# Kernel tuning notes

Measured on AMD Instinct MI355X. Metric: run time of the kernel, lower is better.

Reference implementation:

```python
import jax, jax.numpy as jnp
import numpy as np

N_NODES = 50000
N_EDGES = 1_600_000
T = 2
F_IN = 128
F_OUT = 128


def setup_inputs() -> dict:
    key = jax.random.key(0)
    k1, k2, k3, k4, k5, k6 = jax.random.split(key, 6)
    node_features = jax.random.normal(k1, (N_NODES, T, F_IN), dtype=jnp.float32)
    edge_weights = jax.random.uniform(k2, (T, N_EDGES), dtype=jnp.float32)
    src = jax.random.randint(k3, (N_EDGES,), 0, N_NODES, dtype=jnp.int32)
    dst = jax.random.randint(k4, (N_EDGES,), 0, N_NODES, dtype=jnp.int32)
    W = jax.random.normal(k5, (F_OUT, F_IN), dtype=jnp.float32) / np.sqrt(F_IN)
    b = jax.random.normal(k6, (F_OUT,), dtype=jnp.float32) * 0.01
    return {"node_features": node_features, "edge_weights": edge_weights,
            "src": src, "dst": dst, "W": W, "b": b}


def reference(node_features, edge_weights, src, dst, W, b):
    # DGL: graph.edata['e'] = edge_weights.t().unsqueeze(-1)  -> [E, T, 1]
    w = jnp.transpose(edge_weights)[:, :, None]          # [E, T, 1]
    # u_mul_e: gather src node features, scale by edge weight -> [E, T, F]
    msg = node_features[src] * w
    # sum aggregation at destination nodes -> [N, T, F]
    h = jax.ops.segment_sum(msg, dst, num_segments=node_features.shape[0])
    # Linear(in_features, out_features) with bias
    return jnp.einsum('ntf,of->nto', h, W) + b
```

## Files before the change

kernel.cpp:

```cpp
#include <hip/hip_runtime.h>
#include <hip/hip_bf16.h>
#include <hip/hip_fp16.h>


#define TBLOCK 256
#define CAP 96
#define NGRP 8

typedef unsigned int  uint2_v  __attribute__((ext_vector_type(2)));
typedef float         float4_v __attribute__((ext_vector_type(4)));

#define SWZ(r) ((((r) + ((r) >> 2))) & 7)

__global__ void __launch_bounds__(TBLOCK)
transform_kernel(const float* __restrict__ x, const float* __restrict__ W,
                 __half* __restrict__ y, int nrows) {
    __shared__ float xs[64 * 128];
    __shared__ float Wsh[64 * 128];

    const int tid = threadIdx.x;
    const int tc = tid & 15, tr = tid >> 4;
    const int rowbase = (blockIdx.x >> 1) * 64;
    const int colbase = (blockIdx.x & 1) << 6;

    for (int p = tid; p < 2048; p += TBLOCK) {
        int oL = p >> 5, fb = p & 31;
        *(float4*)&Wsh[oL * 128 + (fb ^ SWZ(oL)) * 4] =
            *(const float4*)&W[((size_t)(colbase + oL)) * 128 + fb * 4];
    }
    for (int p = tid; p < 2048; p += TBLOCK) {
        int r = p >> 5, fb = p & 31;
        int row = rowbase + r;
        float4 v = make_float4(0.f, 0.f, 0.f, 0.f);
        if (row < nrows) v = *(const float4*)&x[(size_t)row * 128 + fb * 4];
        *(float4*)&xs[r * 128 + (fb ^ SWZ(r)) * 4] = v;
    }
    __syncthreads();

    float acc[4][4] = {};
    #pragma unroll 4
    for (int fb = 0; fb < 32; ++fb) {
        float4 a[4], bb[4];
        #pragma unroll
        for (int i = 0; i < 4; ++i) {
            int r = tr + 16 * i;
            a[i] = *(const float4*)&xs[r * 128 + (fb ^ SWZ(r)) * 4];
        }
        #pragma unroll
        for (int j = 0; j < 4; ++j) {
            int oL = 4 * tc + j;
            bb[j] = *(const float4*)&Wsh[oL * 128 + (fb ^ SWZ(oL)) * 4];
        }
        #pragma unroll
        for (int i = 0; i < 4; ++i)
            #pragma unroll
            for (int j = 0; j < 4; ++j)
                acc[i][j] += a[i].x * bb[j].x + a[i].y * bb[j].y
                           + a[i].z * bb[j].z + a[i].w * bb[j].w;
    }

    #pragma unroll
    for (int i = 0; i < 4; ++i) {
        int row = rowbase + tr + 16 * i;
        if (row >= nrows) continue;
        __half2 h0 = __floats2half2_rn(acc[i][0], acc[i][1]);
        __half2 h1 = __floats2half2_rn(acc[i][2], acc[i][3]);
        uint2 pack;
        pack.x = *(unsigned*)&h0;
        pack.y = *(unsigned*)&h1;
        *(uint2*)&y[(size_t)row * 128 + colbase + 4 * tc] = pack;
    }
}

__global__ void __launch_bounds__(TBLOCK)
fill_kernel(const int* __restrict__ src, const int* __restrict__ dst,
            const float* __restrict__ ew, int* __restrict__ cnt,
            unsigned long long* __restrict__ lists, int E, int N) {
    const int g   = blockIdx.x & (NGRP - 1);
    const int bs  = blockIdx.x >> 3;
    const int B   = gridDim.x >> 3;
    const int per = (N + NGRP - 1) / NGRP;
    const int lo  = g * per;
    const unsigned span = (unsigned)((N - lo) < per ? (N - lo) : per);

    for (int e = bs * TBLOCK + (int)threadIdx.x; e < E; e += B * TBLOCK) {
        int d = dst[e];
        if ((unsigned)(d - lo) < span) {
            int pos = atomicAdd(&cnt[d], 1);
            if (pos < CAP) {
                __half2 hw = __floats2half2_rn(ew[e], ew[(size_t)E + e]);
                unsigned long long ent =
                    (unsigned long long)(unsigned)src[e] |
                    ((unsigned long long)(*(unsigned*)&hw) << 32);
                lists[(size_t)d * CAP + pos] = ent;
            }
        }
    }
}

__global__ void __launch_bounds__(TBLOCK)
pull_kernel(const __half* __restrict__ y, const int* __restrict__ cnt,
            const unsigned long long* __restrict__ lists,
            const float* __restrict__ b, float* __restrict__ out, int N) {
    int wid = blockIdx.x * 4 + __builtin_amdgcn_readfirstlane(threadIdx.x >> 6);
    if (wid >= N) return;
    const int lane = threadIdx.x & 63;
    const bool hi = lane >= 32;

    const uint2* yv = (const uint2*)y;
    float4 acc = ((const float4*)b)[lane & 31];

    int c = cnt[wid];
    if (c > CAP) c = CAP;
    const unsigned long long* lp = lists + (size_t)wid * CAP;
    int i = 0;

    #define ACCUM(ee, rr) do {                                            \
        unsigned wbits = (unsigned)((ee) >> 32);                          \
        __half2 w2 = *(__half2*)&wbits;                                   \
        float aw = __half2float(hi ? __high2half(w2) : __low2half(w2));   \
        float2 f0 = __half22float2(*(const __half2*)&(rr).x);             \
        float2 f1 = __half22float2(*(const __half2*)&(rr).y);             \
        acc.x += aw * f0.x; acc.y += aw * f0.y;                           \
        acc.z += aw * f1.x; acc.w += aw * f1.y; } while (0)

    for (; i + 3 < c; i += 4) {
        unsigned long long e0 = __builtin_nontemporal_load(&lp[i]);
        unsigned long long e1 = __builtin_nontemporal_load(&lp[i + 1]);
        unsigned long long e2 = __builtin_nontemporal_load(&lp[i + 2]);
        unsigned long long e3 = __builtin_nontemporal_load(&lp[i + 3]);
        uint2 r0 = yv[(size_t)(unsigned)e0 * 64 + lane];
        uint2 r1 = yv[(size_t)(unsigned)e1 * 64 + lane];
        uint2 r2 = yv[(size_t)(unsigned)e2 * 64 + lane];
        uint2 r3 = yv[(size_t)(unsigned)e3 * 64 + lane];
        ACCUM(e0, r0); ACCUM(e1, r1); ACCUM(e2, r2); ACCUM(e3, r3);
    }
    for (; i < c; ++i) {
        unsigned long long e = __builtin_nontemporal_load(&lp[i]);
        uint2 r = yv[(size_t)(unsigned)e * 64 + lane];
        ACCUM(e, r);
    }

    float4_v av; av.x = acc.x; av.y = acc.y; av.z = acc.z; av.w = acc.w;
    __builtin_nontemporal_store(av, (float4_v*)&((float4*)out)[(size_t)wid * 64 + lane]);
}

extern "C" void kernel_launch(void* const* d_in, const int* in_sizes, int n_in,
                              void* d_out, int out_size, void* d_ws, size_t ws_size,
                              hipStream_t stream) {
    const float* x   = (const float*)d_in[0];
    const float* ew  = (const float*)d_in[1];
    const int*   src = (const int*)d_in[2];
    const int*   dst = (const int*)d_in[3];
    const float* W   = (const float*)d_in[4];
    const float* b   = (const float*)d_in[5];
    float* out = (float*)d_out;

    const int E     = in_sizes[2];
    const int nrows = in_sizes[0] / 128;
    const int N     = nrows / 2;

    char* w8 = (char*)d_ws;
    __half* y  = (__half*)w8;  w8 += (size_t)nrows * 128 * sizeof(__half);
    int* cnt   = (int*)w8;     w8 += (size_t)N * sizeof(int);
    w8 = (char*)(((uintptr_t)w8 + 15) & ~(uintptr_t)15);
    unsigned long long* lists = (unsigned long long*)w8;

    {
        int tiles_r = (nrows + 63) / 64;
        transform_kernel<<<tiles_r * 2, TBLOCK, 0, stream>>>(x, W, y, nrows);
    }

    (void)hipMemsetAsync(cnt, 0, (size_t)N * sizeof(int), stream);
    fill_kernel<<<NGRP * 192, TBLOCK, 0, stream>>>(src, dst, ew, cnt, lists, E, N);

    pull_kernel<<<(N + 3) / 4, TBLOCK, 0, stream>>>(y, cnt, lists, b, out, N);
}
```

Measured before the change: 260.4 us.

## Use fp16 MFMA for node transform and fold counter zeroing into it

The dense per-node linear transform moves from FP32 scalar FMAs on two column-half tiles to MFMA 16x16x32 fp16 instructions, with each block covering all 128 outputs for 64 rows. Inputs and W are converted to fp16 on load into XOR-swizzled LDS. The separate memset of the per-node edge counters is removed, and the transform kernel now zeroes them. This lowers matrix-op cost and saves a launch, but it rounds x and W to fp16 before multiplying, and the zeroing is correct only while the grid covers N.

Measured after the change: 211.4 us. 1.23x faster.

```diff
diff --git a/kernel.cpp b/kernel.cpp
--- a/kernel.cpp
+++ b/kernel.cpp
@@ -7,68 +7,82 @@
 #define CAP 96
 #define NGRP 8
 
-typedef unsigned int  uint2_v  __attribute__((ext_vector_type(2)));
-typedef float         float4_v __attribute__((ext_vector_type(4)));
-
-#define SWZ(r) ((((r) + ((r) >> 2))) & 7)
+typedef _Float16 half8 __attribute__((ext_vector_type(8)));
+typedef float    f32x4 __attribute__((ext_vector_type(4)));
+typedef float    float4_v __attribute__((ext_vector_type(4)));
 
 __global__ void __launch_bounds__(TBLOCK)
 transform_kernel(const float* __restrict__ x, const float* __restrict__ W,
-                 __half* __restrict__ y, int nrows) {
-    __shared__ float xs[64 * 128];
-    __shared__ float Wsh[64 * 128];
+                 __half* __restrict__ y, int* __restrict__ cnt, int Ncnt,
+                 int nrows) {
+    __shared__ _Float16 Wl[128 * 128];
+    __shared__ _Float16 xl[64 * 128];
 
     const int tid = threadIdx.x;
-    const int tc = tid & 15, tr = tid >> 4;
-    const int rowbase = (blockIdx.x >> 1) * 64;
-    const int colbase = (blockIdx.x & 1) << 6;
+    const int rowbase = blockIdx.x * 64;
+
+    int gid = blockIdx.x * TBLOCK + tid;
+    if (gid < Ncnt) cnt[gid] = 0;
 
     for (int p = tid; p < 2048; p += TBLOCK) {
-        int oL = p >> 5, fb = p & 31;
-        *(float4*)&Wsh[oL * 128 + (fb ^ SWZ(oL)) * 4] =
-            *(const float4*)&W[((size_t)(colbase + oL)) * 128 + fb * 4];
+        int o = p >> 4, ch = p & 15;
+        const float4* g = (const float4*)&W[(size_t)o * 128 + ch * 8];
+        float4 u0 = g[0], u1 = g[1];
+        half8 h;
+        h[0] = (_Float16)u0.x; h[1] = (_Float16)u0.y;
+        h[2] = (_Float16)u0.z; h[3] = (_Float16)u0.w;
+        h[4] = (_Float16)u1.x; h[5] = (_Float16)u1.y;
+        h[6] = (_Float16)u1.z; h[7] = (_Float16)u1.w;
+        *(half8*)&Wl[o * 128 + ((ch ^ (o & 7)) << 3)] = h;
     }
-    for (int p = tid; p < 2048; p += TBLOCK) {
-        int r = p >> 5, fb = p & 31;
+    for (int p = tid; p < 1024; p += TBLOCK) {
+        int r = p >> 4, ch = p & 15;
         int row = rowbase + r;
-        float4 v = make_float4(0.f, 0.f, 0.f, 0.f);
-        if (row < nrows) v = *(const float4*)&x[(size_t)row * 128 + fb * 4];
-        *(float4*)&xs[r * 128 + (fb ^ SWZ(r)) * 4] = v;
+        half8 h = {};
+        if (row < nrows) {
+            const float4* g = (const float4*)&x[(size_t)row * 128 + ch * 8];
+            float4 u0 = g[0], u1 = g[1];
+            h[0] = (_Float16)u0.x; h[1] = (_Float16)u0.y;
+            h[2] = (_Float16)u0.z; h[3] = (_Float16)u0.w;
+            h[4] = (_Float16)u1.x; h[5] = (_Float16)u1.y;
+            h[6] = (_Float16)u1.z; h[7] = (_Float16)u1.w;
+        }
+        *(half8*)&xl[r * 128 + ((ch ^ (r & 7)) << 3)] = h;
     }
     __syncthreads();
 
-    float acc[4][4] = {};
-    #pragma unroll 4
-    for (int fb = 0; fb < 32; ++fb) {
-        float4 a[4], bb[4];
+    const int l    = tid & 63;
+    const int wv   = tid >> 6;
+    const int rloc = wv * 16 + (l & 15);
+    const int kg   = (l >> 4);
+
+    half8 xf[4];
+    #pragma unroll
+    for (int s = 0; s < 4; ++s)
+        xf[s] = *(const half8*)&xl[rloc * 128 + (((s * 4 + kg) ^ (rloc & 7)) << 3)];
+
+    f32x4 acc[8] = {};
+    #pragma unroll
+    for (int s = 0; s < 4; ++s) {
         #pragma unroll
-        for (int i = 0; i < 4; ++i) {
-            int r = tr + 16 * i;
-            a[i] = *(const float4*)&xs[r * 128 + (fb ^ SWZ(r)) * 4];
+        for (int c = 0; c < 8; ++c) {
+            int o = c * 16 + (l & 15);
+            half8 wf = *(const half8*)&Wl[o * 128 + (((s * 4 + kg) ^ (o & 7)) << 3)];
+            acc[c] = __builtin_amdgcn_mfma_f32_16x16x32_f16(wf, xf[s], acc[c], 0, 0, 0);
         }
-        #pragma unroll
-        for (int j = 0; j < 4; ++j) {
-            int oL = 4 * tc + j;
-            bb[j] = *(const float4*)&Wsh[oL * 128 + (fb ^ SWZ(oL)) * 4];
-        }
-        #pragma unroll
-        for (int i = 0; i < 4; ++i)
-            #pragma unroll
-            for (int j = 0; j < 4; ++j)
-                acc[i][j] += a[i].x * bb[j].x + a[i].y * bb[j].y
-                           + a[i].z * bb[j].z + a[i].w * bb[j].w;
     }
 
-    #pragma unroll
-    for (int i = 0; i < 4; ++i) {
-        int row = rowbase + tr + 16 * i;
-        if (row >= nrows) continue;
-        __half2 h0 = __floats2half2_rn(acc[i][0], acc[i][1]);
-        __half2 h1 = __floats2half2_rn(acc[i][2], acc[i][3]);
-        uint2 pack;
-        pack.x = *(unsigned*)&h0;
-        pack.y = *(unsigned*)&h1;
-        *(uint2*)&y[(size_t)row * 128 + colbase + 4 * tc] = pack;
+    const int row = rowbase + rloc;
+    if (row < nrows) {
+        #pragma unroll
+        for (int c = 0; c < 8; ++c) {
+            __half2 h0 = __floats2half2_rn(acc[c][0], acc[c][1]);
+            __half2 h1 = __floats2half2_rn(acc[c][2], acc[c][3]);
+            uint2 pk;
+            pk.x = *(unsigned*)&h0;
+            pk.y = *(unsigned*)&h1;
+            *(uint2*)&y[(size_t)row * 128 + c * 16 + kg * 4] = pk;
+        }
     }
 }
 
@@ -168,10 +182,9 @@
 
     {
         int tiles_r = (nrows + 63) / 64;
-        transform_kernel<<<tiles_r * 2, TBLOCK, 0, stream>>>(x, W, y, nrows);
+        transform_kernel<<<tiles_r, TBLOCK, 0, stream>>>(x, W, y, cnt, N, nrows);
     }
 
-    (void)hipMemsetAsync(cnt, 0, (size_t)N * sizeof(int), stream);
     fill_kernel<<<NGRP * 192, TBLOCK, 0, stream>>>(src, dst, ew, cnt, lists, E, N);
 
     pull_kernel<<<(N + 3) / 4, TBLOCK, 0, stream>>>(y, cnt, lists, b, out, N);
```
